# Performance work log

Hardware: AMD Instinct MI355X
Metric: run time of the kernel (lower is better)

The kernel has to match this reference:

```python
import jax, jax.numpy as jnp
import numpy as np

NL = 2    # num_layers
H = 4     # attention heads
C = 512   # hidden_dim
IN = 256  # in_dim
F = 16    # fanout
B = 256   # seed nodes
NC = 47   # num_classes
DH = C // H
EPS = 1e-5


def _ln(x, g, b):
    mu = jnp.mean(x, -1, keepdims=True)
    var = jnp.mean((x - mu) ** 2, -1, keepdims=True)
    return (x - mu) * jax.lax.rsqrt(var + EPS) * g + b


def _mha(x, wqkv, bqkv, wo, bo):
    # torch nn.MultiheadAttention with a single batch of N tokens
    n = x.shape[0]
    qkv = x @ wqkv.T + bqkv                      # [N, 3C]
    q, k, v = jnp.split(qkv, 3, axis=-1)
    q = q.reshape(n, H, DH).transpose(1, 0, 2)   # [H, N, DH]
    k = k.reshape(n, H, DH).transpose(1, 0, 2)
    v = v.reshape(n, H, DH).transpose(1, 0, 2)
    s = jnp.einsum('hnd,hmd->hnm', q, k) * (1.0 / float(np.sqrt(DH)))
    a = jax.nn.softmax(s, axis=-1)
    o = jnp.einsum('hnm,hmd->hnd', a, v).transpose(1, 0, 2).reshape(n, C)
    return o @ wo.T + bo


def setup_inputs() -> dict:
    ks = jax.random.split(jax.random.key(0), 16)
    n = [B, B * F, B * F * F]
    p = lambda i, shape: jax.random.normal(ks[i], shape, jnp.float32) * 0.02
    return {
        'feats0': jax.random.normal(ks[0], (n[0], IN), jnp.float32),
        'feats1': jax.random.normal(ks[1], (n[1], IN), jnp.float32),
        'feats2': jax.random.normal(ks[2], (n[2], IN), jnp.float32),
        'nmask0': jnp.ones((n[0],), jnp.float32),
        'nmask1': jnp.ones((n[1],), jnp.float32),
        'nmask2': jnp.ones((n[2],), jnp.float32),
        'nbmask0': jax.random.randint(ks[3], (n[0], F), 0, 2, jnp.int32),
        'nbmask1': jax.random.randint(ks[4], (n[1], F), 0, 2, jnp.int32),
        'emb_w': p(5, (C, IN)), 'emb_b': jnp.zeros((C,), jnp.float32),
        'sage_w': p(6, (NL, C, 2 * C)), 'sage_b': jnp.zeros((NL, C), jnp.float32),
        'qkv_w': p(7, (NL, 3 * C, C)), 'qkv_b': jnp.zeros((NL, 3 * C), jnp.float32),
        'out_w': p(8, (NL, C, C)), 'out_b': jnp.zeros((NL, C), jnp.float32),
        'n1_g': jnp.ones((NL, C), jnp.float32), 'n1_b': jnp.zeros((NL, C), jnp.float32),
        'n2_g': jnp.ones((NL, C), jnp.float32), 'n2_b': jnp.zeros((NL, C), jnp.float32),
        'ffn_w1': p(9, (NL, 2 * C, C)), 'ffn_b1': jnp.zeros((NL, 2 * C), jnp.float32),
        'ffn_w2': p(10, (NL, C, 2 * C)), 'ffn_b2': jnp.zeros((NL, C), jnp.float32),
        'cls_w': p(11, (NC, C)), 'cls_b': jnp.zeros((NC,), jnp.float32),
    }


def reference(feats0, feats1, feats2, nmask0, nmask1, nmask2, nbmask0, nbmask1,
              emb_w, emb_b, sage_w, sage_b, qkv_w, qkv_b, out_w, out_b,
              n1_g, n1_b, n2_g, n2_b, ffn_w1, ffn_b1, ffn_w2, ffn_b2, cls_w, cls_b):
    nmasks = [nmask0, nmask1, nmask2]
    nbm = [nbmask0.astype(jnp.float32), nbmask1.astype(jnp.float32)]
    # embedding + node-mask gating per depth
    states = [(f @ emb_w.T + emb_b) * m[:, None]
              for f, m in zip([feats0, feats1, feats2], nmasks)]
    for li in range(NL):
        prev = states
        nxt = list(prev)
        for depth in range(NL - li - 1, -1, -1):
            # masked mean aggregation of sampled neighbors: [n_d, F, C] -> [n_d, C]
            child = prev[depth + 1].reshape(-1, F, C)
            m = nbm[depth][:, :, None]
            summed = jnp.sum(child * m, axis=1)
            denom = jnp.clip(jnp.sum(m, axis=1), 1.0)
            agg = summed / denom
            sf = prev[depth]
            # GraphSAGE concat update (no activation, dropout=0)
            h_local = jnp.concatenate([sf, agg], -1) @ sage_w[li].T + sage_b[li]
            h = _ln(sf + h_local, n1_g[li], n1_b[li])
            h = _ln(h + _mha(h, qkv_w[li], qkv_b[li], out_w[li], out_b[li]),
                    n2_g[li], n2_b[li])
            hf = jax.nn.relu(h @ ffn_w1[li].T + ffn_b1[li]) @ ffn_w2[li].T + ffn_b2[li]
            nxt[depth] = (h + hf) * nmasks[depth][:, None]
        states = nxt
    return states[0] @ cls_w.T + cls_b
```

## Files before the change

kernel.cpp:

```cpp
#include <hip/hip_runtime.h>
#include <math.h>


typedef unsigned short bf16_t;
typedef __attribute__((ext_vector_type(8))) short bf16x8_t;
typedef __attribute__((ext_vector_type(4))) float f32x4_t;

__device__ __forceinline__ bf16_t f2bf(float f) {
  union { float f; unsigned u; } v; v.f = f;
  unsigned r = v.u + 0x7FFFu + ((v.u >> 16) & 1u);
  return (bf16_t)(r >> 16);
}
__device__ __forceinline__ float bf2f(bf16_t u) {
  union { unsigned u; float f; } v; v.u = ((unsigned)u) << 16; return v.f;
}
__device__ __forceinline__ unsigned cvtpk(float lo, float hi) {
  unsigned r;
  asm("v_cvt_pk_bf16_f32 %0, %1, %2" : "=v"(r) : "v"(lo), "v"(hi));
  return r;
}
__device__ __forceinline__ void gload16(const void* g, void* l) {
  __builtin_amdgcn_global_load_lds(
      (const __attribute__((address_space(1))) unsigned int*)g,
      (__attribute__((address_space(3))) unsigned int*)l, 16, 0, 0);
}

#define QSCALE (0.08838834764831845f * 1.4426950408889634f)

template <int BM, int BN, int MODE, bool SPLIT>
__global__ __launch_bounds__(256) void mgemm(
    const bf16_t* __restrict__ A, const bf16_t* __restrict__ A2,
    const bf16_t* __restrict__ W, const float* __restrict__ bias,
    const bf16_t* __restrict__ res, const float* __restrict__ rowa,
    const float* __restrict__ rowb,
    bf16_t* __restrict__ Cb, bf16_t* __restrict__ Vt,
    int M, int N, int K) {
  constexpr int FM = BM / 32, FN = BN / 32;
  constexpr int NCH = (BM + BN) / 16;
  constexpr int CPW = NCH / 4;
  __shared__ bf16_t lds[2][(BM + BN) * 32];
  const int t = threadIdx.x;
  const int w = t >> 6, lane = t & 63;
  const int g = lane >> 4, li = lane & 15;
  const int bm = blockIdx.x * BM, bn = blockIdx.y * BN;
  const int wr = (w >> 1) * (BM / 2), wc = (w & 1) * (BN / 2);
  f32x4_t acc[FM][FN] = {};

  auto stage = [&](int buf, int k0) {
#pragma unroll
    for (int c0 = 0; c0 < CPW; ++c0) {
      const int c = w * CPW + c0;
      const int row = c * 16 + (lane >> 2);
      const int gk = k0 + (lane & 3) * 8;
      const bf16_t* src;
      if (row < BM) {
        if (SPLIT) {
          src = (gk < 512) ? (A + (size_t)(bm + row) * 512 + gk)
                           : (A2 + (size_t)(bm + row) * 512 + (gk - 512));
        } else {
          src = A + (size_t)(bm + row) * K + gk;
        }
      } else {
        src = W + (size_t)(bn + row - BM) * K + gk;
      }
      gload16(src, &lds[buf][c * 512]);
    }
  };

  const int nk = K / 32;
  stage(0, 0);
  for (int ks = 0; ks < nk; ++ks) {
    __syncthreads();
    if (ks + 1 < nk) stage((ks + 1) & 1, (ks + 1) * 32);
    const bf16_t* As = &lds[ks & 1][0];
    const bf16_t* Bs = &lds[ks & 1][BM * 32];
    bf16x8_t af[FM], bfr[FN];
#pragma unroll
    for (int i = 0; i < FM; ++i)
      af[i] = *(const bf16x8_t*)(As + (wr + i * 16 + li) * 32 + g * 8);
#pragma unroll
    for (int j = 0; j < FN; ++j)
      bfr[j] = *(const bf16x8_t*)(Bs + (wc + j * 16 + li) * 32 + g * 8);
#pragma unroll
    for (int i = 0; i < FM; ++i)
#pragma unroll
      for (int j = 0; j < FN; ++j)
        acc[i][j] = __builtin_amdgcn_mfma_f32_16x16x32_bf16(
            af[i], bfr[j], acc[i][j], 0, 0, 0);
  }

#pragma unroll
  for (int i = 0; i < FM; ++i) {
    const int mb = bm + wr + i * 16 + g * 4;
#pragma unroll
    for (int j = 0; j < FN; ++j) {
      const int n = bn + wc + j * 16 + li;
      if (MODE == 5) {
        const float bb = bias[n];
        if (n < 512) {
#pragma unroll
          for (int r = 0; r < 4; ++r)
            Cb[(size_t)(mb + r) * 1024 + n] = f2bf((acc[i][j][r] + bb) * QSCALE);
        } else if (n < 1024) {
#pragma unroll
          for (int r = 0; r < 4; ++r)
            Cb[(size_t)(mb + r) * 1024 + n] = f2bf(acc[i][j][r] + bb);
        } else {
          ushort4 o;
          o.x = f2bf(acc[i][j][0] + bb); o.y = f2bf(acc[i][j][1] + bb);
          o.z = f2bf(acc[i][j][2] + bb); o.w = f2bf(acc[i][j][3] + bb);
          *(ushort4*)(Vt + (size_t)(n - 1024) * M + mb) = o;
        }
      } else {
#pragma unroll
        for (int r = 0; r < 4; ++r) {
          const int m = mb + r;
          const float v = acc[i][j][r];
          if (MODE == 0) Cb[(size_t)m * N + n] = f2bf(v + bias[n]);
          if (MODE == 1) Cb[(size_t)m * N + n] = f2bf((v + bias[n]) * rowa[m]);
          if (MODE == 2)
            Cb[(size_t)m * N + n] = f2bf((v + bias[n] * rowa[m]) * rowb[m]);
          if (MODE == 3) Cb[(size_t)m * N + n] = f2bf(fmaxf(v + bias[n], 0.f));
          if (MODE == 4)
            Cb[(size_t)m * N + n] =
                f2bf((v + bias[n] + bf2f(res[(size_t)m * N + n])) * rowa[m]);
        }
      }
    }
  }
}

template <int NW, int NQC, int SPLITS>
__global__ __launch_bounds__(NW * 64) void flashT(
    const bf16_t* __restrict__ qk, const bf16_t* __restrict__ vt,
    bf16_t* __restrict__ attno, bf16_t* __restrict__ Ofb,
    float* __restrict__ Ml, int N) {
  constexpr int QB = NW * NQC * 16;
  constexpr int KCH = 16 / NW;
  __shared__ bf16_t Ks[2][64 * 128];
  __shared__ bf16_t Vs[2][128 * 64];
  __shared__ bf16_t Ps[NW][16 * 64];
  const int bid = blockIdx.x;
  const int sp = bid % SPLITS;
  const int h = (bid / SPLITS) & 3;
  const int qb = bid / (4 * SPLITS);
  const int t = threadIdx.x, w = t >> 6, lane = t & 63;
  const int g = lane >> 4, li = lane & 15;
  const int kvbase = sp * (N / SPLITS);
  const int nt = (N / SPLITS) >> 6;

  bf16x8_t qf[NQC][4];
#pragma unroll
  for (int qc = 0; qc < NQC; ++qc) {
    const bf16_t* qrow =
        qk + (size_t)(qb * QB + w * (NQC * 16) + qc * 16 + li) * 1024 + h * 128;
#pragma unroll
    for (int ks = 0; ks < 4; ++ks)
      qf[qc][ks] = *(const bf16x8_t*)(qrow + ks * 32 + g * 8);
  }

  int koff[4], voff[2], pwoff[4];
#pragma unroll
  for (int ks = 0; ks < 4; ++ks)
    koff[ks] = li * 256 + (((ks * 4 + g) ^ (li & 7)) << 4);
#pragma unroll
  for (int ks = 0; ks < 2; ++ks)
    voff[ks] = li * 128 + (((ks * 4 + g) ^ (li & 7)) << 4);
#pragma unroll
  for (int mf = 0; mf < 4; ++mf)
    pwoff[mf] = li * 128 + (((mf * 2 + (g >> 1)) ^ (li & 7)) << 4) +
                ((g & 1) << 3);
  char* Pb = (char*)Ps + w * 2048;

  const bf16_t* kp[KCH];
  const bf16_t* vp[KCH];
#pragma unroll
  for (int i = 0; i < KCH; ++i) {
    const int c = w * KCH + i;
    const int rk = c * 4 + (lane >> 4);
    kp[i] = qk + (size_t)(kvbase + rk) * 1024 + 512 + h * 128 +
            (((lane & 15) ^ (rk & 7)) * 8);
    const int rv = c * 8 + (lane >> 3);
    vp[i] = vt + (size_t)(h * 128 + rv) * N + kvbase +
            (((lane & 7) ^ (rv & 7)) * 8);
  }
  auto stage = [&](int buf) {
#pragma unroll
    for (int i = 0; i < KCH; ++i) {
      const int c = w * KCH + i;
      gload16(kp[i], &Ks[buf][c * 512]);
      kp[i] += 64 * 1024;
      gload16(vp[i], &Vs[buf][c * 512]);
      vp[i] += 64;
    }
  };

  f32x4_t acc[NQC][8] = {};
  float mrun[NQC], lrun[NQC];
#pragma unroll
  for (int qc = 0; qc < NQC; ++qc) { mrun[qc] = -1e30f; lrun[qc] = 0.f; }

  stage(0);
  for (int tt = 0; tt < nt; ++tt) {
    const int cur = tt & 1;
    __syncthreads();
    if (tt + 1 < nt) stage(cur ^ 1);
    const char* Kb = (const char*)Ks + cur * 16384;
    const char* Vb = (const char*)Vs + cur * 16384;

    f32x4_t sf[NQC][4];
#pragma unroll
    for (int qc = 0; qc < NQC; ++qc)
#pragma unroll
      for (int mf = 0; mf < 4; ++mf) sf[qc][mf] = (f32x4_t){0.f, 0.f, 0.f, 0.f};
    __builtin_amdgcn_s_setprio(1);
#pragma unroll
    for (int ks = 0; ks < 4; ++ks) {
#pragma unroll
      for (int mf = 0; mf < 4; ++mf) {
        const bf16x8_t kf = *(const bf16x8_t*)(Kb + koff[ks] + mf * 4096);
#pragma unroll
        for (int qc = 0; qc < NQC; ++qc)
          sf[qc][mf] = __builtin_amdgcn_mfma_f32_16x16x32_bf16(
              kf, qf[qc][ks], sf[qc][mf], 0, 0, 0);
      }
    }
    __builtin_amdgcn_s_setprio(0);

    float tmax[NQC];
#pragma unroll
    for (int qc = 0; qc < NQC; ++qc) {
      float tm = -1e30f;
#pragma unroll
      for (int mf = 0; mf < 4; ++mf)
#pragma unroll
        for (int r = 0; r < 4; ++r) tm = fmaxf(tm, sf[qc][mf][r]);
      tm = fmaxf(tm, __shfl_xor(tm, 16));
      tm = fmaxf(tm, __shfl_xor(tm, 32));
      tmax[qc] = tm;
    }
    float worst = tmax[0] - mrun[0];
#pragma unroll
    for (int qc = 1; qc < NQC; ++qc)
      worst = fmaxf(worst, tmax[qc] - mrun[qc]);
    if (!__all(worst <= 11.0f)) {
#pragma unroll
      for (int qc = 0; qc < NQC; ++qc) {
        const float mnew = fmaxf(mrun[qc], tmax[qc]);
        const float fsc = exp2f(mrun[qc] - mnew);
        mrun[qc] = mnew;
        lrun[qc] *= fsc;
#pragma unroll
        for (int mf = 0; mf < 8; ++mf) acc[qc][mf] *= fsc;
      }
    }
#pragma unroll
    for (int qc = 0; qc < NQC; ++qc) {
      float lsum = 0.f;
#pragma unroll
      for (int mf = 0; mf < 4; ++mf)
#pragma unroll
        for (int r = 0; r < 4; ++r) {
          const float p = exp2f(sf[qc][mf][r] - mrun[qc]);
          sf[qc][mf][r] = p;
          lsum += p;
        }
      lsum += __shfl_xor(lsum, 16);
      lsum += __shfl_xor(lsum, 32);
      lrun[qc] += lsum;
    }

    __builtin_amdgcn_s_setprio(1);
#pragma unroll
    for (int qc = 0; qc < NQC; ++qc) {
#pragma unroll
      for (int mf = 0; mf < 4; ++mf) {
        uint2 pv;
        pv.x = cvtpk(sf[qc][mf][0], sf[qc][mf][1]);
        pv.y = cvtpk(sf[qc][mf][2], sf[qc][mf][3]);
        *(uint2*)(Pb + pwoff[mf]) = pv;
      }
#pragma unroll
      for (int ks = 0; ks < 2; ++ks) {
        const bf16x8_t pf = *(const bf16x8_t*)(Pb + voff[ks]);
#pragma unroll
        for (int mf = 0; mf < 8; ++mf) {
          const bf16x8_t vf = *(const bf16x8_t*)(Vb + voff[ks] + mf * 2048);
          acc[qc][mf] = __builtin_amdgcn_mfma_f32_16x16x32_bf16(
              vf, pf, acc[qc][mf], 0, 0, 0);
        }
      }
    }
    __builtin_amdgcn_s_setprio(0);
  }

#pragma unroll
  for (int qc = 0; qc < NQC; ++qc) {
    const float invl = 1.f / lrun[qc];
    const int q = qb * QB + w * (NQC * 16) + qc * 16 + li;
    bf16_t* dst = (SPLITS == 1) ? (attno + (size_t)q * 512 + h * 128)
                                : (Ofb + ((size_t)sp * N + q) * 512 + h * 128);
#pragma unroll
    for (int mf = 0; mf < 8; ++mf) {
      ushort4 o;
      o.x = f2bf(acc[qc][mf][0] * invl); o.y = f2bf(acc[qc][mf][1] * invl);
      o.z = f2bf(acc[qc][mf][2] * invl); o.w = f2bf(acc[qc][mf][3] * invl);
      *(ushort4*)(dst + mf * 16 + g * 4) = o;
    }
    if (SPLITS > 1 && lane < 16) {
      float2 ml; ml.x = mrun[qc]; ml.y = lrun[qc];
      *(float2*)(Ml + ((size_t)(sp * 4 + h) * N + q) * 2) = ml;
    }
  }
}

template <int SPLITS>
__global__ __launch_bounds__(256) void merge_attn(
    const bf16_t* __restrict__ Ofb, const float* __restrict__ Ml,
    bf16_t* __restrict__ attno, int N) {
  const int q = blockIdx.x, t = threadIdx.x;
#pragma unroll
  for (int half = 0; half < 2; ++half) {
    const int c = t + half * 256;
    const int h = c >> 7;
    float2 ml[SPLITS];
    float m = -1e30f;
#pragma unroll
    for (int s = 0; s < SPLITS; ++s) {
      ml[s] = ((const float2*)Ml)[(s * 4 + h) * N + q];
      m = fmaxf(m, ml[s].x);
    }
    float num = 0.f, den = 0.f;
#pragma unroll
    for (int s = 0; s < SPLITS; ++s) {
      const float wgt = ml[s].y * exp2f(ml[s].x - m);
      num += bf2f(Ofb[((size_t)s * N + q) * 512 + c]) * wgt;
      den += wgt;
    }
    attno[(size_t)q * 512 + c] = f2bf(num / den);
  }
}

__global__ __launch_bounds__(256) void add_ln(
    const bf16_t* __restrict__ X, const bf16_t* __restrict__ Y,
    const float* __restrict__ gg, const float* __restrict__ bb,
    bf16_t* __restrict__ out) {
  const int row = blockIdx.x, t = threadIdx.x;
  const size_t base = (size_t)row * 512;
  const float x0 = bf2f(X[base + t]) + bf2f(Y[base + t]);
  const float x1 = bf2f(X[base + 256 + t]) + bf2f(Y[base + 256 + t]);
  float s = x0 + x1, ss = x0 * x0 + x1 * x1;
#pragma unroll
  for (int o = 32; o > 0; o >>= 1) {
    s += __shfl_down(s, o);
    ss += __shfl_down(ss, o);
  }
  __shared__ float rs[4], rss[4], sm[2];
  const int wv = t >> 6, ln = t & 63;
  if (ln == 0) { rs[wv] = s; rss[wv] = ss; }
  __syncthreads();
  if (t == 0) {
    const float S = rs[0] + rs[1] + rs[2] + rs[3];
    const float SS = rss[0] + rss[1] + rss[2] + rss[3];
    const float mean = S * (1.f / 512.f);
    sm[0] = mean;
    sm[1] = rsqrtf(SS * (1.f / 512.f) - mean * mean + 1e-5f);
  }
  __syncthreads();
  const float mean = sm[0], rstd = sm[1];
  out[base + t] = f2bf((x0 - mean) * rstd * gg[t] + bb[t]);
  out[base + 256 + t] = f2bf((x1 - mean) * rstd * gg[t + 256] + bb[t + 256]);
}

__global__ __launch_bounds__(256) void agg_feats(
    const float* __restrict__ feats2, const int* __restrict__ nbm,
    const float* __restrict__ nm2, bf16_t* __restrict__ aggF,
    float* __restrict__ sw, float* __restrict__ invd) {
  const int node = blockIdx.x * 4 + (threadIdx.x >> 6);
  const int lane = threadIdx.x & 63;
  float4 acc = {0.f, 0.f, 0.f, 0.f};
  float ws = 0.f, nbs = 0.f;
#pragma unroll
  for (int j = 0; j < 16; ++j) {
    const float nb = (float)nbm[node * 16 + j];
    const float wj = nb * nm2[node * 16 + j];
    const float4 v =
        *(const float4*)(feats2 + (size_t)(node * 16 + j) * 256 + lane * 4);
    acc.x += wj * v.x; acc.y += wj * v.y;
    acc.z += wj * v.z; acc.w += wj * v.w;
    ws += wj;
    nbs += nb;
  }
  ushort4 o;
  o.x = f2bf(acc.x); o.y = f2bf(acc.y); o.z = f2bf(acc.z); o.w = f2bf(acc.w);
  *(ushort4*)(aggF + (size_t)node * 256 + lane * 4) = o;
  if (lane == 0) { sw[node] = ws; invd[node] = 1.f / fmaxf(nbs, 1.f); }
}

__global__ __launch_bounds__(256) void agg_state(
    const bf16_t* __restrict__ src, const int* __restrict__ nbm,
    bf16_t* __restrict__ agg) {
  const int i = blockIdx.x, t = threadIdx.x;
  float a0 = 0.f, a1 = 0.f, nbs = 0.f;
#pragma unroll
  for (int j = 0; j < 16; ++j) {
    const float nb = (float)nbm[i * 16 + j];
    const bf16_t* r = src + (size_t)(i * 16 + j) * 512;
    a0 += nb * bf2f(r[t]);
    a1 += nb * bf2f(r[t + 256]);
    nbs += nb;
  }
  const float inv = 1.f / fmaxf(nbs, 1.f);
  agg[(size_t)i * 512 + t] = f2bf(a0 * inv);
  agg[(size_t)i * 512 + 256 + t] = f2bf(a1 * inv);
}

__global__ __launch_bounds__(256) void cvt_all(
    const float* __restrict__ s_emb, const float* __restrict__ s_sage,
    const float* __restrict__ s_qkv, const float* __restrict__ s_out,
    const float* __restrict__ s_f1, const float* __restrict__ s_f2,
    const float* __restrict__ s_ft0, const float* __restrict__ s_ft1,
    bf16_t* __restrict__ d_emb, bf16_t* __restrict__ d_sage,
    bf16_t* __restrict__ d_qkv, bf16_t* __restrict__ d_out,
    bf16_t* __restrict__ d_f1, bf16_t* __restrict__ d_f2,
    bf16_t* __restrict__ d_ft0, bf16_t* __restrict__ d_ft1) {
  int i = blockIdx.x * 256 + threadIdx.x;
  const float* s; bf16_t* d; int base;
  if (i < 32768)        { s = s_emb;  d = d_emb;  base = 0; }
  else if (i < 294912)  { s = s_sage; d = d_sage; base = 32768; }
  else if (i < 688128)  { s = s_qkv;  d = d_qkv;  base = 294912; }
  else if (i < 819200)  { s = s_out;  d = d_out;  base = 688128; }
  else if (i < 1081344) { s = s_f1;   d = d_f1;   base = 819200; }
  else if (i < 1343488) { s = s_f2;   d = d_f2;   base = 1081344; }
  else if (i < 1359872) { s = s_ft0;  d = d_ft0;  base = 1343488; }
  else                  { s = s_ft1;  d = d_ft1;  base = 1359872; }
  i -= base;
  const float4 v = ((const float4*)s)[i];
  ushort4 o;
  o.x = f2bf(v.x); o.y = f2bf(v.y); o.z = f2bf(v.z); o.w = f2bf(v.w);
  ((ushort4*)d)[i] = o;
}

__global__ __launch_bounds__(256) void cls_k(
    const bf16_t* __restrict__ s, const float* __restrict__ wc,
    const float* __restrict__ bc, float* __restrict__ out) {
  __shared__ float srow[512];
  const int m = blockIdx.x, t = threadIdx.x;
  srow[t] = bf2f(s[(size_t)m * 512 + t]);
  srow[t + 256] = bf2f(s[(size_t)m * 512 + 256 + t]);
  __syncthreads();
  if (t < 47) {
    float a = bc[t];
    const float* wr = wc + (size_t)t * 512;
    for (int k = 0; k < 512; ++k) a += srow[k] * wr[k];
    out[(size_t)m * 47 + t] = a;
  }
}

struct LayerW {
  const bf16_t *wsage, *wqkv, *wout, *wf1, *wf2;
  const float *bsage, *bqkv, *bout, *bf1, *bf2;
  const float *n1g, *n1b, *n2g, *n2b;
};
struct Scratch {
  bf16_t *tmpb, *h1, *h2, *qkb, *vt, *attno, *f1o, *Ofb;
  float *Ml;
};

static void run_block(int n, const bf16_t* sf, const bf16_t* agg,
                      const float* nmask, const LayerW& L, const Scratch& S,
                      bf16_t* sout, hipStream_t st) {
  if (n == 4096) {
    mgemm<64, 128, 0, true><<<dim3(64, 4), 256, 0, st>>>(
        sf, agg, L.wsage, L.bsage, nullptr, nullptr, nullptr, S.tmpb, nullptr,
        n, 512, 1024);
    add_ln<<<n, 256, 0, st>>>(sf, S.tmpb, L.n1g, L.n1b, S.h1);
    mgemm<128, 128, 5, false><<<dim3(32, 12), 256, 0, st>>>(
        S.h1, nullptr, L.wqkv, L.bqkv, nullptr, nullptr, nullptr,
        S.qkb, S.vt, n, 1536, 512);
    flashT<8, 2, 4><<<(n / 256) * 16, 512, 0, st>>>(S.qkb, S.vt, nullptr,
                                                    S.Ofb, S.Ml, n);
    merge_attn<4><<<n, 256, 0, st>>>(S.Ofb, S.Ml, S.attno, n);
    mgemm<64, 128, 0, false><<<dim3(64, 4), 256, 0, st>>>(
        S.attno, nullptr, L.wout, L.bout, nullptr, nullptr, nullptr, S.tmpb,
        nullptr, n, 512, 512);
    add_ln<<<n, 256, 0, st>>>(S.h1, S.tmpb, L.n2g, L.n2b, S.h2);
    mgemm<128, 128, 3, false><<<dim3(32, 8), 256, 0, st>>>(
        S.h2, nullptr, L.wf1, L.bf1, nullptr, nullptr, nullptr, S.f1o, nullptr,
        n, 1024, 512);
    mgemm<64, 128, 4, false><<<dim3(64, 4), 256, 0, st>>>(
        S.f1o, nullptr, L.wf2, L.bf2, S.h2, nmask, nullptr, sout, nullptr,
        n, 512, 1024);
  } else {
    mgemm<64, 64, 0, true><<<dim3(4, 8), 256, 0, st>>>(
        sf, agg, L.wsage, L.bsage, nullptr, nullptr, nullptr, S.tmpb, nullptr,
        n, 512, 1024);
    add_ln<<<n, 256, 0, st>>>(sf, S.tmpb, L.n1g, L.n1b, S.h1);
    mgemm<64, 64, 5, false><<<dim3(4, 24), 256, 0, st>>>(
        S.h1, nullptr, L.wqkv, L.bqkv, nullptr, nullptr, nullptr,
        S.qkb, S.vt, n, 1536, 512);
    flashT<4, 1, 1><<<(n / 64) * 4, 256, 0, st>>>(S.qkb, S.vt, S.attno,
                                                  nullptr, nullptr, n);
    mgemm<64, 64, 0, false><<<dim3(4, 8), 256, 0, st>>>(
        S.attno, nullptr, L.wout, L.bout, nullptr, nullptr, nullptr, S.tmpb,
        nullptr, n, 512, 512);
    add_ln<<<n, 256, 0, st>>>(S.h1, S.tmpb, L.n2g, L.n2b, S.h2);
    mgemm<64, 64, 3, false><<<dim3(4, 16), 256, 0, st>>>(
        S.h2, nullptr, L.wf1, L.bf1, nullptr, nullptr, nullptr, S.f1o, nullptr,
        n, 1024, 512);
    mgemm<64, 64, 4, false><<<dim3(4, 8), 256, 0, st>>>(
        S.f1o, nullptr, L.wf2, L.bf2, S.h2, nmask, nullptr, sout, nullptr,
        n, 512, 1024);
  }
}

extern "C" void kernel_launch(void* const* d_in, const int* in_sizes, int n_in,
                              void* d_out, int out_size, void* d_ws,
                              size_t ws_size, hipStream_t stream) {
  const float* feats0 = (const float*)d_in[0];
  const float* feats1 = (const float*)d_in[1];
  const float* feats2 = (const float*)d_in[2];
  const float* nmask0 = (const float*)d_in[3];
  const float* nmask1 = (const float*)d_in[4];
  const float* nmask2 = (const float*)d_in[5];
  const int* nbmask0 = (const int*)d_in[6];
  const int* nbmask1 = (const int*)d_in[7];
  const float* emb_w = (const float*)d_in[8];
  const float* emb_b = (const float*)d_in[9];
  const float* sage_w = (const float*)d_in[10];
  const float* sage_b = (const float*)d_in[11];
  const float* qkv_w = (const float*)d_in[12];
  const float* qkv_b = (const float*)d_in[13];
  const float* out_w = (const float*)d_in[14];
  const float* out_b = (const float*)d_in[15];
  const float* n1_g = (const float*)d_in[16];
  const float* n1_b = (const float*)d_in[17];
  const float* n2_g = (const float*)d_in[18];
  const float* n2_b = (const float*)d_in[19];
  const float* ffn_w1 = (const float*)d_in[20];
  const float* ffn_b1 = (const float*)d_in[21];
  const float* ffn_w2 = (const float*)d_in[22];
  const float* ffn_b2 = (const float*)d_in[23];
  const float* cls_w = (const float*)d_in[24];
  const float* cls_b = (const float*)d_in[25];
  float* out = (float*)d_out;

  size_t off = 0;
  auto alloc = [&](size_t bytes) {
    void* r = (char*)d_ws + off;
    off += (bytes + 255) & ~(size_t)255;
    return r;
  };
  bf16_t* wemb = (bf16_t*)alloc((size_t)512 * 256 * 2);
  bf16_t* wsage = (bf16_t*)alloc((size_t)2 * 512 * 1024 * 2);
  bf16_t* wqkv = (bf16_t*)alloc((size_t)2 * 1536 * 512 * 2);
  bf16_t* wout = (bf16_t*)alloc((size_t)2 * 512 * 512 * 2);
  bf16_t* wf1 = (bf16_t*)alloc((size_t)2 * 1024 * 512 * 2);
  bf16_t* wf2 = (bf16_t*)alloc((size_t)2 * 512 * 1024 * 2);
  bf16_t* f0b = (bf16_t*)alloc((size_t)256 * 256 * 2);
  bf16_t* f1b = (bf16_t*)alloc((size_t)4096 * 256 * 2);
  bf16_t* s0 = (bf16_t*)alloc((size_t)256 * 512 * 2);
  bf16_t* s0b = (bf16_t*)alloc((size_t)256 * 512 * 2);
  bf16_t* s0f = (bf16_t*)alloc((size_t)256 * 512 * 2);
  bf16_t* s1 = (bf16_t*)alloc((size_t)4096 * 512 * 2);
  bf16_t* s1b = (bf16_t*)alloc((size_t)4096 * 512 * 2);
  bf16_t* aggFb = (bf16_t*)alloc((size_t)4096 * 256 * 2);
  float* swv = (float*)alloc((size_t)4096 * 4);
  float* invd = (float*)alloc((size_t)4096 * 4);
  bf16_t* aggb = (bf16_t*)alloc((size_t)4096 * 512 * 2);
  bf16_t* tmpb = (bf16_t*)alloc((size_t)4096 * 512 * 2);
  bf16_t* h1 = (bf16_t*)alloc((size_t)4096 * 512 * 2);
  bf16_t* h2 = (bf16_t*)alloc((size_t)4096 * 512 * 2);
  bf16_t* qkb = (bf16_t*)alloc((size_t)4096 * 1024 * 2);
  bf16_t* vt = (bf16_t*)alloc((size_t)512 * 4096 * 2);
  bf16_t* attno = (bf16_t*)alloc((size_t)4096 * 512 * 2);
  bf16_t* f1o = (bf16_t*)alloc((size_t)4096 * 1024 * 2);
  bf16_t* Ofb = (bf16_t*)alloc((size_t)4 * 4096 * 512 * 2);
  float* Ml = (float*)alloc((size_t)4 * 4 * 4096 * 2 * 4);

  cvt_all<<<6336, 256, 0, stream>>>(emb_w, sage_w, qkv_w, out_w, ffn_w1,
                                    ffn_w2, feats0, feats1, wemb, wsage, wqkv,
                                    wout, wf1, wf2, f0b, f1b);

  mgemm<64, 128, 1, false><<<dim3(64, 4), 256, 0, stream>>>(
      f1b, nullptr, wemb, emb_b, nullptr, nmask1, nullptr, s1, nullptr,
      4096, 512, 256);
  mgemm<64, 64, 1, false><<<dim3(4, 8), 256, 0, stream>>>(
      f0b, nullptr, wemb, emb_b, nullptr, nmask0, nullptr, s0, nullptr,
      256, 512, 256);
  agg_feats<<<1024, 256, 0, stream>>>(feats2, nbmask1, nmask2, aggFb, swv, invd);
  mgemm<64, 128, 2, false><<<dim3(64, 4), 256, 0, stream>>>(
      aggFb, nullptr, wemb, emb_b, nullptr, swv, invd, aggb, nullptr,
      4096, 512, 256);

  LayerW L0{wsage, wqkv, wout, wf1, wf2,
            sage_b, qkv_b, out_b, ffn_b1, ffn_b2,
            n1_g, n1_b, n2_g, n2_b};
  LayerW L1{wsage + 512 * 1024, wqkv + 1536 * 512, wout + 512 * 512,
            wf1 + 1024 * 512, wf2 + 512 * 1024,
            sage_b + 512, qkv_b + 1536, out_b + 512, ffn_b1 + 1024,
            ffn_b2 + 512, n1_g + 512, n1_b + 512, n2_g + 512, n2_b + 512};
  Scratch S{tmpb, h1, h2, qkb, vt, attno, f1o, Ofb, Ml};

  run_block(4096, s1, aggb, nmask1, L0, S, s1b, stream);
  agg_state<<<256, 256, 0, stream>>>(s1, nbmask0, aggb);
  run_block(256, s0, aggb, nmask0, L0, S, s0b, stream);
  agg_state<<<256, 256, 0, stream>>>(s1b, nbmask0, aggb);
  run_block(256, s0b, aggb, nmask0, L1, S, s0f, stream);

  cls_k<<<256, 256, 0, stream>>>(s0f, cls_w, cls_b, out);
}
```

Baseline: 310.9 us.

## Batch depth-1 and depth-0 layer-0 blocks into one concatenated row set

Concatenates the 4096 depth-1 rows and 256 depth-0 rows into one 4352-row buffer, so layer 0's embedding, SAGE, QKV, out-projection and FFN GEMMs and layernorms run as single launches. Attention is still run separately per segment, with a new V-stride argument. This removes a full set of small, underutilized launches for the 256-row block. agg_state is also vectorized to one wave per node with 16-byte loads. The GEMM epilogue gains a per-row branch to pick between the two mask arrays, and buffer offsets become more intricate.

```diff
diff --git a/kernel.cpp b/kernel.cpp
--- a/kernel.cpp
+++ b/kernel.cpp
@@ -5,6 +5,9 @@
 typedef unsigned short bf16_t;
 typedef __attribute__((ext_vector_type(8))) short bf16x8_t;
 typedef __attribute__((ext_vector_type(4))) float f32x4_t;
+
+#define M_BIG 4096
+#define M_CAT 4352
 
 __device__ __forceinline__ bf16_t f2bf(float f) {
   union { float f; unsigned u; } v; v.f = f;
@@ -32,9 +35,9 @@
     const bf16_t* __restrict__ A, const bf16_t* __restrict__ A2,
     const bf16_t* __restrict__ W, const float* __restrict__ bias,
     const bf16_t* __restrict__ res, const float* __restrict__ rowa,
-    const float* __restrict__ rowb,
+    const float* __restrict__ rowa2, const float* __restrict__ rowb,
     bf16_t* __restrict__ Cb, bf16_t* __restrict__ Vt,
-    int M, int N, int K) {
+    int M, int M1, int N, int K) {
   constexpr int FM = BM / 32, FN = BN / 32;
   constexpr int NCH = (BM + BN) / 16;
   constexpr int CPW = NCH / 4;
@@ -117,13 +120,18 @@
           const int m = mb + r;
           const float v = acc[i][j][r];
           if (MODE == 0) Cb[(size_t)m * N + n] = f2bf(v + bias[n]);
-          if (MODE == 1) Cb[(size_t)m * N + n] = f2bf((v + bias[n]) * rowa[m]);
+          if (MODE == 1) {
+            const float ra = (m < M1) ? rowa[m] : rowa2[m - M1];
+            Cb[(size_t)m * N + n] = f2bf((v + bias[n]) * ra);
+          }
           if (MODE == 2)
             Cb[(size_t)m * N + n] = f2bf((v + bias[n] * rowa[m]) * rowb[m]);
           if (MODE == 3) Cb[(size_t)m * N + n] = f2bf(fmaxf(v + bias[n], 0.f));
-          if (MODE == 4)
+          if (MODE == 4) {
+            const float ra = (m < M1) ? rowa[m] : rowa2[m - M1];
             Cb[(size_t)m * N + n] =
-                f2bf((v + bias[n] + bf2f(res[(size_t)m * N + n])) * rowa[m]);
+                f2bf((v + bias[n] + bf2f(res[(size_t)m * N + n])) * ra);
+          }
         }
       }
     }
@@ -134,7 +142,7 @@
 __global__ __launch_bounds__(NW * 64) void flashT(
     const bf16_t* __restrict__ qk, const bf16_t* __restrict__ vt,
     bf16_t* __restrict__ attno, bf16_t* __restrict__ Ofb,
-    float* __restrict__ Ml, int N) {
+    float* __restrict__ Ml, int N, int VS) {
   constexpr int QB = NW * NQC * 16;
   constexpr int KCH = 16 / NW;
   __shared__ bf16_t Ks[2][64 * 128];
@@ -181,7 +189,7 @@
     kp[i] = qk + (size_t)(kvbase + rk) * 1024 + 512 + h * 128 +
             (((lane & 15) ^ (rk & 7)) * 8);
     const int rv = c * 8 + (lane >> 3);
-    vp[i] = vt + (size_t)(h * 128 + rv) * N + kvbase +
+    vp[i] = vt + (size_t)(h * 128 + rv) * VS + kvbase +
             (((lane & 7) ^ (rv & 7)) * 8);
   }
   auto stage = [&](int buf) {
@@ -400,19 +408,24 @@
 __global__ __launch_bounds__(256) void agg_state(
     const bf16_t* __restrict__ src, const int* __restrict__ nbm,
     bf16_t* __restrict__ agg) {
-  const int i = blockIdx.x, t = threadIdx.x;
-  float a0 = 0.f, a1 = 0.f, nbs = 0.f;
+  const int node = blockIdx.x * 4 + (threadIdx.x >> 6);
+  const int lane = threadIdx.x & 63;
+  float acc[8] = {};
+  float nbs = 0.f;
 #pragma unroll
   for (int j = 0; j < 16; ++j) {
-    const float nb = (float)nbm[i * 16 + j];
-    const bf16_t* r = src + (size_t)(i * 16 + j) * 512;
-    a0 += nb * bf2f(r[t]);
-    a1 += nb * bf2f(r[t + 256]);
+    const float nb = (float)nbm[node * 16 + j];
     nbs += nb;
+    const bf16x8_t v =
+        *(const bf16x8_t*)(src + (size_t)(node * 16 + j) * 512 + lane * 8);
+#pragma unroll
+    for (int e = 0; e < 8; ++e) acc[e] += nb * bf2f((bf16_t)v[e]);
   }
   const float inv = 1.f / fmaxf(nbs, 1.f);
-  agg[(size_t)i * 512 + t] = f2bf(a0 * inv);
-  agg[(size_t)i * 512 + 256 + t] = f2bf(a1 * inv);
+  bf16x8_t o;
+#pragma unroll
+  for (int e = 0; e < 8; ++e) o[e] = (short)f2bf(acc[e] * inv);
+  *(bf16x8_t*)(agg + (size_t)node * 512 + lane * 8) = o;
 }
 
 __global__ __launch_bounds__(256) void cvt_all(
@@ -454,63 +467,6 @@
     const float* wr = wc + (size_t)t * 512;
     for (int k = 0; k < 512; ++k) a += srow[k] * wr[k];
     out[(size_t)m * 47 + t] = a;
-  }
-}
-
-struct LayerW {
-  const bf16_t *wsage, *wqkv, *wout, *wf1, *wf2;
-  const float *bsage, *bqkv, *bout, *bf1, *bf2;
-  const float *n1g, *n1b, *n2g, *n2b;
-};
-struct Scratch {
-  bf16_t *tmpb, *h1, *h2, *qkb, *vt, *attno, *f1o, *Ofb;
-  float *Ml;
-};
-
-static void run_block(int n, const bf16_t* sf, const bf16_t* agg,
-                      const float* nmask, const LayerW& L, const Scratch& S,
-                      bf16_t* sout, hipStream_t st) {
-  if (n == 4096) {
-    mgemm<64, 128, 0, true><<<dim3(64, 4), 256, 0, st>>>(
-        sf, agg, L.wsage, L.bsage, nullptr, nullptr, nullptr, S.tmpb, nullptr,
-        n, 512, 1024);
-    add_ln<<<n, 256, 0, st>>>(sf, S.tmpb, L.n1g, L.n1b, S.h1);
-    mgemm<128, 128, 5, false><<<dim3(32, 12), 256, 0, st>>>(
-        S.h1, nullptr, L.wqkv, L.bqkv, nullptr, nullptr, nullptr,
-        S.qkb, S.vt, n, 1536, 512);
-    flashT<8, 2, 4><<<(n / 256) * 16, 512, 0, st>>>(S.qkb, S.vt, nullptr,
-                                                    S.Ofb, S.Ml, n);
-    merge_attn<4><<<n, 256, 0, st>>>(S.Ofb, S.Ml, S.attno, n);
-    mgemm<64, 128, 0, false><<<dim3(64, 4), 256, 0, st>>>(
-        S.attno, nullptr, L.wout, L.bout, nullptr, nullptr, nullptr, S.tmpb,
-        nullptr, n, 512, 512);
-    add_ln<<<n, 256, 0, st>>>(S.h1, S.tmpb, L.n2g, L.n2b, S.h2);
-    mgemm<128, 128, 3, false><<<dim3(32, 8), 256, 0, st>>>(
-        S.h2, nullptr, L.wf1, L.bf1, nullptr, nullptr, nullptr, S.f1o, nullptr,
-        n, 1024, 512);
-    mgemm<64, 128, 4, false><<<dim3(64, 4), 256, 0, st>>>(
-        S.f1o, nullptr, L.wf2, L.bf2, S.h2, nmask, nullptr, sout, nullptr,
-        n, 512, 1024);
-  } else {
-    mgemm<64, 64, 0, true><<<dim3(4, 8), 256, 0, st>>>(
-        sf, agg, L.wsage, L.bsage, nullptr, nullptr, nullptr, S.tmpb, nullptr,
-        n, 512, 1024);
-    add_ln<<<n, 256, 0, st>>>(sf, S.tmpb, L.n1g, L.n1b, S.h1);
-    mgemm<64, 64, 5, false><<<dim3(4, 24), 256, 0, st>>>(
-        S.h1, nullptr, L.wqkv, L.bqkv, nullptr, nullptr, nullptr,
-        S.qkb, S.vt, n, 1536, 512);
-    flashT<4, 1, 1><<<(n / 64) * 4, 256, 0, st>>>(S.qkb, S.vt, S.attno,
-                                                  nullptr, nullptr, n);
-    mgemm<64, 64, 0, false><<<dim3(4, 8), 256, 0, st>>>(
-        S.attno, nullptr, L.wout, L.bout, nullptr, nullptr, nullptr, S.tmpb,
-        nullptr, n, 512, 512);
-    add_ln<<<n, 256, 0, st>>>(S.h1, S.tmpb, L.n2g, L.n2b, S.h2);
-    mgemm<64, 64, 3, false><<<dim3(4, 16), 256, 0, st>>>(
-        S.h2, nullptr, L.wf1, L.bf1, nullptr, nullptr, nullptr, S.f1o, nullptr,
-        n, 1024, 512);
-    mgemm<64, 64, 4, false><<<dim3(4, 8), 256, 0, st>>>(
-        S.f1o, nullptr, L.wf2, L.bf2, S.h2, nmask, nullptr, sout, nullptr,
-        n, 512, 1024);
   }
 }
 
@@ -557,56 +513,91 @@
   bf16_t* wout = (bf16_t*)alloc((size_t)2 * 512 * 512 * 2);
   bf16_t* wf1 = (bf16_t*)alloc((size_t)2 * 1024 * 512 * 2);
   bf16_t* wf2 = (bf16_t*)alloc((size_t)2 * 512 * 1024 * 2);
-  bf16_t* f0b = (bf16_t*)alloc((size_t)256 * 256 * 2);
-  bf16_t* f1b = (bf16_t*)alloc((size_t)4096 * 256 * 2);
-  bf16_t* s0 = (bf16_t*)alloc((size_t)256 * 512 * 2);
-  bf16_t* s0b = (bf16_t*)alloc((size_t)256 * 512 * 2);
-  bf16_t* s0f = (bf16_t*)alloc((size_t)256 * 512 * 2);
-  bf16_t* s1 = (bf16_t*)alloc((size_t)4096 * 512 * 2);
-  bf16_t* s1b = (bf16_t*)alloc((size_t)4096 * 512 * 2);
+  bf16_t* fcat = (bf16_t*)alloc((size_t)M_CAT * 256 * 2);
+  bf16_t* s_cat = (bf16_t*)alloc((size_t)M_CAT * 512 * 2);
+  bf16_t* scat_o = (bf16_t*)alloc((size_t)M_CAT * 512 * 2);
+  bf16_t* agg_cat = (bf16_t*)alloc((size_t)M_CAT * 512 * 2);
   bf16_t* aggFb = (bf16_t*)alloc((size_t)4096 * 256 * 2);
   float* swv = (float*)alloc((size_t)4096 * 4);
   float* invd = (float*)alloc((size_t)4096 * 4);
-  bf16_t* aggb = (bf16_t*)alloc((size_t)4096 * 512 * 2);
-  bf16_t* tmpb = (bf16_t*)alloc((size_t)4096 * 512 * 2);
-  bf16_t* h1 = (bf16_t*)alloc((size_t)4096 * 512 * 2);
-  bf16_t* h2 = (bf16_t*)alloc((size_t)4096 * 512 * 2);
-  bf16_t* qkb = (bf16_t*)alloc((size_t)4096 * 1024 * 2);
-  bf16_t* vt = (bf16_t*)alloc((size_t)512 * 4096 * 2);
-  bf16_t* attno = (bf16_t*)alloc((size_t)4096 * 512 * 2);
-  bf16_t* f1o = (bf16_t*)alloc((size_t)4096 * 1024 * 2);
+  bf16_t* agg256 = (bf16_t*)alloc((size_t)256 * 512 * 2);
+  bf16_t* s0f = (bf16_t*)alloc((size_t)256 * 512 * 2);
+  bf16_t* tmpb = (bf16_t*)alloc((size_t)M_CAT * 512 * 2);
+  bf16_t* h1 = (bf16_t*)alloc((size_t)M_CAT * 512 * 2);
+  bf16_t* h2 = (bf16_t*)alloc((size_t)M_CAT * 512 * 2);
+  bf16_t* qkb = (bf16_t*)alloc((size_t)M_CAT * 1024 * 2);
+  bf16_t* vt = (bf16_t*)alloc((size_t)512 * M_CAT * 2);
+  bf16_t* attno = (bf16_t*)alloc((size_t)M_CAT * 512 * 2);
+  bf16_t* f1o = (bf16_t*)alloc((size_t)M_CAT * 1024 * 2);
   bf16_t* Ofb = (bf16_t*)alloc((size_t)4 * 4096 * 512 * 2);
   float* Ml = (float*)alloc((size_t)4 * 4 * 4096 * 2 * 4);
 
   cvt_all<<<6336, 256, 0, stream>>>(emb_w, sage_w, qkv_w, out_w, ffn_w1,
                                     ffn_w2, feats0, feats1, wemb, wsage, wqkv,
-                                    wout, wf1, wf2, f0b, f1b);
-
-  mgemm<64, 128, 1, false><<<dim3(64, 4), 256, 0, stream>>>(
-      f1b, nullptr, wemb, emb_b, nullptr, nmask1, nullptr, s1, nullptr,
-      4096, 512, 256);
-  mgemm<64, 64, 1, false><<<dim3(4, 8), 256, 0, stream>>>(
-      f0b, nullptr, wemb, emb_b, nullptr, nmask0, nullptr, s0, nullptr,
-      256, 512, 256);
+                                    wout, wf1, wf2, fcat + (size_t)4096 * 256,
+                                    fcat);
+
+  mgemm<64, 128, 1, false><<<dim3(M_CAT / 64, 4), 256, 0, stream>>>(
+      fcat, nullptr, wemb, emb_b, nullptr, nmask1, nmask0, nullptr, s_cat,
+      nullptr, M_CAT, M_BIG, 512, 256);
   agg_feats<<<1024, 256, 0, stream>>>(feats2, nbmask1, nmask2, aggFb, swv, invd);
   mgemm<64, 128, 2, false><<<dim3(64, 4), 256, 0, stream>>>(
-      aggFb, nullptr, wemb, emb_b, nullptr, swv, invd, aggb, nullptr,
-      4096, 512, 256);
-
-  LayerW L0{wsage, wqkv, wout, wf1, wf2,
-            sage_b, qkv_b, out_b, ffn_b1, ffn_b2,
-            n1_g, n1_b, n2_g, n2_b};
-  LayerW L1{wsage + 512 * 1024, wqkv + 1536 * 512, wout + 512 * 512,
-            wf1 + 1024 * 512, wf2 + 512 * 1024,
-            sage_b + 512, qkv_b + 1536, out_b + 512, ffn_b1 + 1024,
-            ffn_b2 + 512, n1_g + 512, n1_b + 512, n2_g + 512, n2_b + 512};
-  Scratch S{tmpb, h1, h2, qkb, vt, attno, f1o, Ofb, Ml};
-
-  run_block(4096, s1, aggb, nmask1, L0, S, s1b, stream);
-  agg_state<<<256, 256, 0, stream>>>(s1, nbmask0, aggb);
-  run_block(256, s0, aggb, nmask0, L0, S, s0b, stream);
-  agg_state<<<256, 256, 0, stream>>>(s1b, nbmask0, aggb);
-  run_block(256, s0b, aggb, nmask0, L1, S, s0f, stream);
+      aggFb, nullptr, wemb, emb_b, nullptr, swv, swv, invd, agg_cat, nullptr,
+      M_BIG, M_BIG, 512, 256);
+  agg_state<<<64, 256, 0, stream>>>(s_cat, nbmask0,
+                                    agg_cat + (size_t)M_BIG * 512);
+
+  mgemm<64, 128, 0, true><<<dim3(M_CAT / 64, 4), 256, 0, stream>>>(
+      s_cat, agg_cat, wsage, sage_b, nullptr, nullptr, nullptr, nullptr, tmpb,
+      nullptr, M_CAT, 0, 512, 1024);
+  add_ln<<<M_CAT, 256, 0, stream>>>(s_cat, tmpb, n1_g, n1_b, h1);
+  mgemm<128, 128, 5, false><<<dim3(M_CAT / 128, 12), 256, 0, stream>>>(
+      h1, nullptr, wqkv, qkv_b, nullptr, nullptr, nullptr, nullptr, qkb, vt,
+      M_CAT, 0, 1536, 512);
+  flashT<8, 2, 4><<<(M_BIG / 256) * 16, 512, 0, stream>>>(
+      qkb, vt, nullptr, Ofb, Ml, M_BIG, M_CAT);
+  flashT<4, 1, 1><<<(256 / 64) * 4, 256, 0, stream>>>(
+      qkb + (size_t)M_BIG * 1024, vt + M_BIG, attno + (size_t)M_BIG * 512,
+      nullptr, nullptr, 256, M_CAT);
+  merge_attn<4><<<M_BIG, 256, 0, stream>>>(Ofb, Ml, attno, M_BIG);
+  mgemm<64, 128, 0, false><<<dim3(M_CAT / 64, 4), 256, 0, stream>>>(
+      attno, nullptr, wout, out_b, nullptr, nullptr, nullptr, nullptr, tmpb,
+      nullptr, M_CAT, 0, 512, 512);
+  add_ln<<<M_CAT, 256, 0, stream>>>(h1, tmpb, n2_g, n2_b, h2);
+  mgemm<128, 128, 3, false><<<dim3(M_CAT / 128, 8), 256, 0, stream>>>(
+      h2, nullptr, wf1, ffn_b1, nullptr, nullptr, nullptr, nullptr, f1o,
+      nullptr, M_CAT, 0, 1024, 512);
+  mgemm<64, 128, 4, false><<<dim3(M_CAT / 64, 4), 256, 0, stream>>>(
+      f1o, nullptr, wf2, ffn_b2, h2, nmask1, nmask0, nullptr, scat_o, nullptr,
+      M_CAT, M_BIG, 512, 1024);
+
+  const bf16_t* s1b = scat_o;
+  const bf16_t* s0b = scat_o + (size_t)M_BIG * 512;
+  agg_state<<<64, 256, 0, stream>>>(s1b, nbmask0, agg256);
+  const bf16_t* wsage1 = wsage + 512 * 1024;
+  const bf16_t* wqkv1 = wqkv + 1536 * 512;
+  const bf16_t* wout1 = wout + 512 * 512;
+  const bf16_t* wf11 = wf1 + 1024 * 512;
+  const bf16_t* wf21 = wf2 + 512 * 1024;
+  mgemm<64, 64, 0, true><<<dim3(4, 8), 256, 0, stream>>>(
+      s0b, agg256, wsage1, sage_b + 512, nullptr, nullptr, nullptr, nullptr,
+      tmpb, nullptr, 256, 0, 512, 1024);
+  add_ln<<<256, 256, 0, stream>>>(s0b, tmpb, n1_g + 512, n1_b + 512, h1);
+  mgemm<64, 64, 5, false><<<dim3(4, 24), 256, 0, stream>>>(
+      h1, nullptr, wqkv1, qkv_b + 1536, nullptr, nullptr, nullptr, nullptr,
+      qkb, vt, 256, 0, 1536, 512);
+  flashT<4, 1, 1><<<(256 / 64) * 4, 256, 0, stream>>>(
+      qkb, vt, attno, nullptr, nullptr, 256, 256);
+  mgemm<64, 64, 0, false><<<dim3(4, 8), 256, 0, stream>>>(
+      attno, nullptr, wout1, out_b + 512, nullptr, nullptr, nullptr, nullptr,
+      tmpb, nullptr, 256, 0, 512, 512);
+  add_ln<<<256, 256, 0, stream>>>(h1, tmpb, n2_g + 512, n2_b + 512, h2);
+  mgemm<64, 64, 3, false><<<dim3(4, 16), 256, 0, stream>>>(
+      h2, nullptr, wf11, ffn_b1 + 1024, nullptr, nullptr, nullptr, nullptr,
+      f1o, nullptr, 256, 0, 1024, 512);
+  mgemm<64, 64, 4, false><<<dim3(4, 8), 256, 0, stream>>>(
+      f1o, nullptr, wf21, ffn_b2 + 512, h2, nmask0, nmask0, nullptr, s0f,
+      nullptr, 256, 256, 512, 1024);
 
   cls_k<<<256, 256, 0, stream>>>(s0f, cls_w, cls_b, out);
 }
```

Result: faster. 261.9 us (-15.8%).
